# Optimization experiments

Measured on AMD Instinct MI355X. Metric: run time of the kernel, lower is better.

Reference implementation:

```python
import jax, jax.numpy as jnp
import numpy as np


def soft_threshold24(w):
    """2:4 soft-threshold along the last dim: in each contiguous group of 4,
    zero the two smallest magnitudes and shrink the two largest by the
    second-smallest magnitude (sign(w) * relu(|w| - t))."""
    M, N = w.shape
    g = w.reshape(M, N // 4, 4)
    a = jnp.abs(g)
    thr = jnp.sort(a, axis=-1)[..., 1:2]  # 2nd-smallest magnitude per group
    s = jnp.sign(g) * jnp.maximum(a - thr, 0.0)
    return s.reshape(M, N)


def mm_fp16(a, b):
    """fake_fp8_mm: cast operands to fp16, accumulate in fp32."""
    return jnp.matmul(a.astype(jnp.float16), b.astype(jnp.float16),
                      preferred_element_type=jnp.float32)


def setup_inputs() -> dict:
    key = jax.random.key(0)
    k0, k1, k2, k3 = jax.random.split(key, 4)
    B, S, D, R = 4, 2048, 2048, 512
    return {
        "x": jax.random.normal(k0, (B, S, D), jnp.float32),
        "weight_in": jax.random.normal(k1, (D, R), jnp.float32) * 0.02,
        "weight_out": jax.random.normal(k2, (D, R), jnp.float32) * 0.02,
        "bias": jax.random.normal(k3, (D,), jnp.float32) * 0.01,
        "sparse_scale_in": jnp.array(1.0, jnp.float32),
        "sparse_scale_out": jnp.array(1.0, jnp.float32),
    }


def reference(x, weight_in, weight_out, bias, sparse_scale_in, sparse_scale_out):
    B, S, D = x.shape
    # stage 1: x @ sparse24(weight_in) * scale_in  -> [B,S,R]
    win_s = soft_threshold24(weight_in) * sparse_scale_in          # [D, R]
    h = mm_fp16(x.reshape(-1, D), win_s)                            # [B*S, R] fp32
    # stage 2: h @ sparse24(weight_out.T) * scale_out + bias -> [B,S,D]
    wout_s = soft_threshold24(weight_out.T) * sparse_scale_out      # [R, D]
    out = mm_fp16(h, wout_s) + bias                                 # [B*S, D]
    return out.reshape(B, S, D)
```

## Files before the change

kernel.cpp:

```cpp
#include <hip/hip_runtime.h>

typedef _Float16 f16;
typedef _Float16 f16x8 __attribute__((ext_vector_type(8)));
typedef float f32x4 __attribute__((ext_vector_type(4)));

#define BK 32

__device__ __forceinline__ void g2l16(const f16* g, f16* l) {
    __builtin_amdgcn_global_load_lds(
        (const __attribute__((address_space(1))) void*)g,
        (__attribute__((address_space(3))) void*)l, 16, 0, 0);
}

template <int N> __device__ __forceinline__ void wait_vmcnt();
template <> __device__ __forceinline__ void wait_vmcnt<0>() { asm volatile("s_waitcnt vmcnt(0)" ::: "memory"); }
template <> __device__ __forceinline__ void wait_vmcnt<3>() { asm volatile("s_waitcnt vmcnt(3)" ::: "memory"); }
template <> __device__ __forceinline__ void wait_vmcnt<4>() { asm volatile("s_waitcnt vmcnt(4)" ::: "memory"); }

__device__ __forceinline__ float soft1(float a, float thr, float w, float s) {
    return copysignf(fmaxf(a - thr, 0.0f), w) * s;
}

__device__ __forceinline__ float thr4(float a0, float a1, float a2, float a3) {
    float lo01 = fminf(a0, a1), hi01 = fmaxf(a0, a1);
    float lo23 = fminf(a2, a3), hi23 = fmaxf(a2, a3);
    return fminf(fmaxf(lo01, lo23), fminf(hi01, hi23));
}

__global__ __launch_bounds__(256) void prep_kernel(
    const float* __restrict__ x, f16* __restrict__ xh, int n8,
    const float* __restrict__ Wi, f16* __restrict__ winT, const float* __restrict__ sci,
    const float* __restrict__ Wo, f16* __restrict__ woutT, const float* __restrict__ sco,
    int D, int R, int nCastB, int nSpInB)
{
    int b = blockIdx.x;
    int tid = threadIdx.x;
    if (b < nCastB) {
        int i = b * 256 + tid;
        if (i < n8) {
            float4 a = reinterpret_cast<const float4*>(x)[2 * i];
            float4 c = reinterpret_cast<const float4*>(x)[2 * i + 1];
            f16x8 o = {(f16)a.x, (f16)a.y, (f16)a.z, (f16)a.w,
                       (f16)c.x, (f16)c.y, (f16)c.z, (f16)c.w};
            reinterpret_cast<f16x8*>(xh)[i] = o;
        }
    } else if (b < nCastB + nSpInB) {
        int t = (b - nCastB) * 256 + tid;
        int RG = R >> 2;
        if (t >= RG * D) return;
        int rg = t / D, d = t - rg * D;
        float s = *sci;
        float4 w = *reinterpret_cast<const float4*>(Wi + (size_t)d * R + rg * 4);
        float a0 = fabsf(w.x), a1 = fabsf(w.y), a2 = fabsf(w.z), a3 = fabsf(w.w);
        float thr = thr4(a0, a1, a2, a3);
        size_t base = (size_t)(rg * 4) * D + d;
        winT[base]                 = (f16)soft1(a0, thr, w.x, s);
        winT[base + D]             = (f16)soft1(a1, thr, w.y, s);
        winT[base + 2 * (size_t)D] = (f16)soft1(a2, thr, w.z, s);
        winT[base + 3 * (size_t)D] = (f16)soft1(a3, thr, w.w, s);
    } else {
        int t = (b - nCastB - nSpInB) * 256 + tid;
        if (t >= (D >> 2) * R) return;
        int dg = t / R, r = t - dg * R;
        float s = *sco;
        size_t i0 = (size_t)(dg * 4) * R + r;
        float w0 = Wo[i0], w1 = Wo[i0 + R], w2 = Wo[i0 + 2 * (size_t)R], w3 = Wo[i0 + 3 * (size_t)R];
        float a0 = fabsf(w0), a1 = fabsf(w1), a2 = fabsf(w2), a3 = fabsf(w3);
        float thr = thr4(a0, a1, a2, a3);
        woutT[i0]                 = (f16)soft1(a0, thr, w0, s);
        woutT[i0 + R]             = (f16)soft1(a1, thr, w1, s);
        woutT[i0 + 2 * (size_t)R] = (f16)soft1(a2, thr, w2, s);
        woutT[i0 + 3 * (size_t)R] = (f16)soft1(a3, thr, w3, s);
    }
}

template <int TBM, int TBN, typename OT, bool BIAS>
__global__ __launch_bounds__(256) void gemm_bt(
    const f16* __restrict__ A, const f16* __restrict__ Bt, OT* __restrict__ C,
    const float* __restrict__ bias, int M, int N, int K)
{
    constexpr int MI = TBM / 32;
    constexpr int NF = TBN / 32;
    constexpr int HM = TBM / 2;
    constexpr int HN = TBN / 2;
    constexpr int L  = TBM / 64 + TBN / 64;
    __shared__ f16 As[2][TBM * BK];
    __shared__ f16 Bs[2][TBN * BK];

    const int tid  = threadIdx.x;
    const int lane = tid & 63;
    const int w    = tid >> 6;
    const int wm   = w & 1;
    const int wn   = w >> 1;
    const int l16  = lane & 15;
    const int quad = lane >> 4;

    const int nbx = N / TBN;
    const int nb  = gridDim.x;
    int d = blockIdx.x;
    int wgid = ((nb & 7) == 0) ? ((d & 7) * (nb >> 3) + (d >> 3)) : d;
    int by = wgid / nbx;
    int bx = wgid - by * nbx;
    const int bm = by * TBM;
    const int bn = bx * TBN;

    const int srow = lane >> 2;
    const int scol = (lane & 3) * 8;
    const f16* gA = A  + (size_t)(bm + w * (TBM / 4) + srow) * K + scol;
    const f16* gB = Bt + (size_t)(bn + w * (TBN / 4) + srow) * K + scol;

    f32x4 acc[MI][NF] = {};

    auto STAGE = [&](int buf, int t) {
        const int k0 = t * BK;
        f16* lA = &As[buf][(w * (TBM / 4)) * BK];
        f16* lB = &Bs[buf][(w * (TBN / 4)) * BK];
#pragma unroll
        for (int i = 0; i < TBM / 64; ++i)
            g2l16(gA + k0 + i * 16 * (size_t)K, lA + i * 16 * BK);
#pragma unroll
        for (int i = 0; i < TBN / 64; ++i)
            g2l16(gB + k0 + i * 16 * (size_t)K, lB + i * 16 * BK);
    };

    auto LOADFRAG = [&](int buf, f16x8* af, f16x8* bf) {
#pragma unroll
        for (int m = 0; m < MI; ++m)
            af[m] = *reinterpret_cast<const f16x8*>(
                &As[buf][(wm * HM + m * 16 + l16) * BK + quad * 8]);
#pragma unroll
        for (int n = 0; n < NF; ++n)
            bf[n] = *reinterpret_cast<const f16x8*>(
                &Bs[buf][(wn * HN + n * 16 + l16) * BK + quad * 8]);
    };

    auto MFMA_ALL = [&](f16x8* af, f16x8* bf) {
#pragma unroll
        for (int m = 0; m < MI; ++m)
#pragma unroll
            for (int n = 0; n < NF; ++n)
                acc[m][n] = __builtin_amdgcn_mfma_f32_16x16x32_f16(af[m], bf[n], acc[m][n], 0, 0, 0);
    };

    const int nk = K / BK;
    STAGE(0, 0);
    STAGE(1, 1);
    for (int t = 0; t < nk - 2; ++t) {
        wait_vmcnt<L>();
        __builtin_amdgcn_s_barrier();
        __builtin_amdgcn_sched_barrier(0);
        f16x8 af[MI], bf[NF];
        LOADFRAG(t & 1, af, bf);
        asm volatile("s_waitcnt lgkmcnt(0)" ::: "memory");
        __builtin_amdgcn_sched_barrier(0);
        __builtin_amdgcn_s_barrier();
        STAGE(t & 1, t + 2);
        MFMA_ALL(af, bf);
    }
    {
        wait_vmcnt<L>();
        __builtin_amdgcn_s_barrier();
        __builtin_amdgcn_sched_barrier(0);
        f16x8 af[MI], bf[NF];
        LOADFRAG(nk & 1, af, bf);
        MFMA_ALL(af, bf);
    }
    {
        wait_vmcnt<0>();
        __builtin_amdgcn_s_barrier();
        __builtin_amdgcn_sched_barrier(0);
        f16x8 af[MI], bf[NF];
        LOADFRAG((nk - 1) & 1, af, bf);
        MFMA_ALL(af, bf);
    }

#pragma unroll
    for (int m = 0; m < MI; ++m) {
        int row_base = bm + wm * HM + m * 16 + quad * 4;
#pragma unroll
        for (int n = 0; n < NF; ++n) {
            int col = bn + wn * HN + n * 16 + l16;
            float b = BIAS ? bias[col] : 0.0f;
#pragma unroll
            for (int r = 0; r < 4; ++r) {
                float v = acc[m][n][r];
                size_t idx = (size_t)(row_base + r) * N + col;
                if constexpr (BIAS) C[idx] = (OT)(v + b);
                else                C[idx] = (OT)v;
            }
        }
    }
}

extern "C" void kernel_launch(void* const* d_in, const int* in_sizes, int n_in,
                              void* d_out, int out_size, void* d_ws, size_t ws_size,
                              hipStream_t stream)
{
    const float* x      = (const float*)d_in[0];
    const float* w_in   = (const float*)d_in[1];
    const float* w_out  = (const float*)d_in[2];
    const float* bias   = (const float*)d_in[3];
    const float* sc_in  = (const float*)d_in[4];
    const float* sc_out = (const float*)d_in[5];

    const int D = in_sizes[3];
    const int R = in_sizes[1] / D;
    const int M = in_sizes[0] / D;

    f16* winT  = (f16*)d_ws;
    f16* woutT = winT + (size_t)R * D;
    f16* h     = woutT + (size_t)D * R;
    f16* xh    = h + (size_t)M * R;
    float* out = (float*)d_out;

    const int n8 = M * D / 8;
    const int nCastB  = (n8 + 255) / 256;
    const int nSpInB  = ((R / 4) * D + 255) / 256;
    const int nSpOutB = ((D / 4) * R + 255) / 256;
    prep_kernel<<<nCastB + nSpInB + nSpOutB, 256, 0, stream>>>(
        x, xh, n8, w_in, winT, sc_in, w_out, woutT, sc_out, D, R, nCastB, nSpInB);

    gemm_bt<64, 128, f16, false><<<(R / 128) * (M / 64), 256, 0, stream>>>(
        xh, winT, h, nullptr, M, R, D);
    gemm_bt<128, 128, float, true><<<(D / 128) * (M / 128), 256, 0, stream>>>(
        h, woutT, out, bias, M, D, R);
}
```

Measured before the change: 178.0 us.

## Fuse fp32-to-fp16 cast of x into first GEMM's LDS fragment loads

Drops the separate pass that casts x to fp16 in the prep kernel. The first GEMM now streams fp32 x tiles straight into LDS with an XOR swizzle and converts them to fp16 when loading fragments. This avoids writing and re-reading a 16M-element fp16 copy of x, at the cost of doubling LDS traffic and footprint for the A tile and adding conversion instructions in the inner loop.

Measured after the change: 197.6 us. +11.0%, slower.

```diff
diff --git a/kernel.cpp b/kernel.cpp
--- a/kernel.cpp
+++ b/kernel.cpp
@@ -6,7 +6,7 @@
 
 #define BK 32
 
-__device__ __forceinline__ void g2l16(const f16* g, f16* l) {
+__device__ __forceinline__ void g2l16(const void* g, void* l) {
     __builtin_amdgcn_global_load_lds(
         (const __attribute__((address_space(1))) void*)g,
         (__attribute__((address_space(3))) void*)l, 16, 0, 0);
@@ -14,7 +14,6 @@
 
 template <int N> __device__ __forceinline__ void wait_vmcnt();
 template <> __device__ __forceinline__ void wait_vmcnt<0>() { asm volatile("s_waitcnt vmcnt(0)" ::: "memory"); }
-template <> __device__ __forceinline__ void wait_vmcnt<3>() { asm volatile("s_waitcnt vmcnt(3)" ::: "memory"); }
 template <> __device__ __forceinline__ void wait_vmcnt<4>() { asm volatile("s_waitcnt vmcnt(4)" ::: "memory"); }
 
 __device__ __forceinline__ float soft1(float a, float thr, float w, float s) {
@@ -28,24 +27,14 @@
 }
 
 __global__ __launch_bounds__(256) void prep_kernel(
-    const float* __restrict__ x, f16* __restrict__ xh, int n8,
     const float* __restrict__ Wi, f16* __restrict__ winT, const float* __restrict__ sci,
     const float* __restrict__ Wo, f16* __restrict__ woutT, const float* __restrict__ sco,
-    int D, int R, int nCastB, int nSpInB)
+    int D, int R, int nSpInB)
 {
     int b = blockIdx.x;
     int tid = threadIdx.x;
-    if (b < nCastB) {
-        int i = b * 256 + tid;
-        if (i < n8) {
-            float4 a = reinterpret_cast<const float4*>(x)[2 * i];
-            float4 c = reinterpret_cast<const float4*>(x)[2 * i + 1];
-            f16x8 o = {(f16)a.x, (f16)a.y, (f16)a.z, (f16)a.w,
-                       (f16)c.x, (f16)c.y, (f16)c.z, (f16)c.w};
-            reinterpret_cast<f16x8*>(xh)[i] = o;
-        }
-    } else if (b < nCastB + nSpInB) {
-        int t = (b - nCastB) * 256 + tid;
+    if (b < nSpInB) {
+        int t = b * 256 + tid;
         int RG = R >> 2;
         if (t >= RG * D) return;
         int rg = t / D, d = t - rg * D;
@@ -59,7 +48,7 @@
         winT[base + 2 * (size_t)D] = (f16)soft1(a2, thr, w.z, s);
         winT[base + 3 * (size_t)D] = (f16)soft1(a3, thr, w.w, s);
     } else {
-        int t = (b - nCastB - nSpInB) * 256 + tid;
+        int t = (b - nSpInB) * 256 + tid;
         if (t >= (D >> 2) * R) return;
         int dg = t / R, r = t - dg * R;
         float s = *sco;
@@ -74,17 +63,21 @@
     }
 }
 
-template <int TBM, int TBN, typename OT, bool BIAS>
+template <int TBM, int TBN, typename AT, typename OT, bool BIAS>
 __global__ __launch_bounds__(256) void gemm_bt(
-    const f16* __restrict__ A, const f16* __restrict__ Bt, OT* __restrict__ C,
+    const AT* __restrict__ A, const f16* __restrict__ Bt, OT* __restrict__ C,
     const float* __restrict__ bias, int M, int N, int K)
 {
+    constexpr bool AF32 = sizeof(AT) == 4;
     constexpr int MI = TBM / 32;
     constexpr int NF = TBN / 32;
     constexpr int HM = TBM / 2;
     constexpr int HN = TBN / 2;
-    constexpr int L  = TBM / 64 + TBN / 64;
-    __shared__ f16 As[2][TBM * BK];
+    constexpr int LA = TBM * BK * (int)sizeof(AT) / 4096;
+    constexpr int LB = TBN * BK * 2 / 4096;
+    constexpr int L  = LA + LB;
+    static_assert(L == 4, "wait_vmcnt<L> instantiations assume L==4");
+    __shared__ AT  As[2][TBM * BK];
     __shared__ f16 Bs[2][TBN * BK];
 
     const int tid  = threadIdx.x;
@@ -106,28 +99,52 @@
 
     const int srow = lane >> 2;
     const int scol = (lane & 3) * 8;
-    const f16* gA = A  + (size_t)(bm + w * (TBM / 4) + srow) * K + scol;
     const f16* gB = Bt + (size_t)(bn + w * (TBN / 4) + srow) * K + scol;
+
+    const int srowA = AF32 ? (lane >> 3) : srow;
+    const int scolA = AF32 ? (((lane & 7) ^ (lane >> 3)) * 4) : scol;
+    const AT* gA = A + (size_t)(bm + w * (TBM / 4) + srowA) * K + scolA;
 
     f32x4 acc[MI][NF] = {};
 
     auto STAGE = [&](int buf, int t) {
         const int k0 = t * BK;
-        f16* lA = &As[buf][(w * (TBM / 4)) * BK];
+        AT*  lA = &As[buf][(w * (TBM / 4)) * BK];
         f16* lB = &Bs[buf][(w * (TBN / 4)) * BK];
-#pragma unroll
-        for (int i = 0; i < TBM / 64; ++i)
-            g2l16(gA + k0 + i * 16 * (size_t)K, lA + i * 16 * BK);
-#pragma unroll
-        for (int i = 0; i < TBN / 64; ++i)
+        if constexpr (AF32) {
+#pragma unroll
+            for (int i = 0; i < (TBM / 4) / 8; ++i)
+                g2l16(gA + k0 + i * 8 * (size_t)K, lA + i * 8 * BK);
+        } else {
+#pragma unroll
+            for (int i = 0; i < (TBM / 4) / 16; ++i)
+                g2l16(gA + k0 + i * 16 * (size_t)K, lA + i * 16 * BK);
+        }
+#pragma unroll
+        for (int i = 0; i < (TBN / 4) / 16; ++i)
             g2l16(gB + k0 + i * 16 * (size_t)K, lB + i * 16 * BK);
     };
 
     auto LOADFRAG = [&](int buf, f16x8* af, f16x8* bf) {
-#pragma unroll
-        for (int m = 0; m < MI; ++m)
-            af[m] = *reinterpret_cast<const f16x8*>(
-                &As[buf][(wm * HM + m * 16 + l16) * BK + quad * 8]);
+        if constexpr (AF32) {
+#pragma unroll
+            for (int m = 0; m < MI; ++m) {
+                int lr = wm * HM + m * 16 + l16;
+                const char* row = reinterpret_cast<const char*>(&As[buf][lr * BK]);
+                int swz = (lr & 7) << 4;
+                f32x4 lo = *reinterpret_cast<const f32x4*>(row + (((quad * 32)      ) ^ swz));
+                f32x4 hi = *reinterpret_cast<const f32x4*>(row + (((quad * 32) + 16 ) ^ swz));
+                f16x8 a;
+#pragma unroll
+                for (int j = 0; j < 4; ++j) { a[j] = (f16)lo[j]; a[j + 4] = (f16)hi[j]; }
+                af[m] = a;
+            }
+        } else {
+#pragma unroll
+            for (int m = 0; m < MI; ++m)
+                af[m] = *reinterpret_cast<const f16x8*>(
+                    &As[buf][(wm * HM + m * 16 + l16) * BK + quad * 8]);
+        }
 #pragma unroll
         for (int n = 0; n < NF; ++n)
             bf[n] = *reinterpret_cast<const f16x8*>(
@@ -146,7 +163,7 @@
     STAGE(0, 0);
     STAGE(1, 1);
     for (int t = 0; t < nk - 2; ++t) {
-        wait_vmcnt<L>();
+        wait_vmcnt<4>();
         __builtin_amdgcn_s_barrier();
         __builtin_amdgcn_sched_barrier(0);
         f16x8 af[MI], bf[NF];
@@ -158,7 +175,7 @@
         MFMA_ALL(af, bf);
     }
     {
-        wait_vmcnt<L>();
+        wait_vmcnt<4>();
         __builtin_amdgcn_s_barrier();
         __builtin_amdgcn_sched_barrier(0);
         f16x8 af[MI], bf[NF];
@@ -210,18 +227,15 @@
     f16* winT  = (f16*)d_ws;
     f16* woutT = winT + (size_t)R * D;
     f16* h     = woutT + (size_t)D * R;
-    f16* xh    = h + (size_t)M * R;
     float* out = (float*)d_out;
 
-    const int n8 = M * D / 8;
-    const int nCastB  = (n8 + 255) / 256;
     const int nSpInB  = ((R / 4) * D + 255) / 256;
     const int nSpOutB = ((D / 4) * R + 255) / 256;
-    prep_kernel<<<nCastB + nSpInB + nSpOutB, 256, 0, stream>>>(
-        x, xh, n8, w_in, winT, sc_in, w_out, woutT, sc_out, D, R, nCastB, nSpInB);
-
-    gemm_bt<64, 128, f16, false><<<(R / 128) * (M / 64), 256, 0, stream>>>(
-        xh, winT, h, nullptr, M, R, D);
-    gemm_bt<128, 128, float, true><<<(D / 128) * (M / 128), 256, 0, stream>>>(
+    prep_kernel<<<nSpInB + nSpOutB, 256, 0, stream>>>(
+        w_in, winT, sc_in, w_out, woutT, sc_out, D, R, nSpInB);
+
+    gemm_bt<64, 128, float, f16, false><<<(R / 128) * (M / 64), 256, 0, stream>>>(
+        x, winT, h, nullptr, M, R, D);
+    gemm_bt<128, 128, f16, float, true><<<(D / 128) * (M / 128), 256, 0, stream>>>(
         h, woutT, out, bias, M, D, R);
 }
```
